# Kernel optimization log

Hardware: AMD Instinct MI355X
Metric: run time of the kernel (lower is better)

The kernel has to match this reference:

```python
import jax, jax.numpy as jnp
import numpy as np

B, IN_CH, OUT_CH, K, W_DIM, H = 16, 512, 512, 3, 512, 32


def setup_inputs() -> dict:
    key = jax.random.key(0)
    k1, k2, k3, k4 = jax.random.split(key, 4)
    return {
        "x": jax.random.normal(k1, (B, IN_CH, H, H), dtype=jnp.float32),
        "w": jax.random.normal(k2, (B, W_DIM), dtype=jnp.float32),
        "weight": jax.random.normal(k3, (1, OUT_CH, IN_CH, K, K), dtype=jnp.float32),
        "lin_w": jax.random.normal(k4, (IN_CH, W_DIM), dtype=jnp.float32),
        "lin_b": jnp.zeros((IN_CH,), dtype=jnp.float32),
    }


def reference(x, w, weight, lin_w, lin_b):
    k = weight.shape[-1]
    in_ch = weight.shape[2]
    fan_in = in_ch * k * k
    # equalized lr scaling of conv weight
    wt = weight * np.float32(np.sqrt(2.0 / fan_in))  # (1, out, in, k, k)
    # EqualizedLinear style: s = w @ (lin_w * sqrt(2/w_dim)).T + b
    s = w @ (lin_w * np.float32(np.sqrt(2.0 / lin_w.shape[1]))).T + lin_b  # (B, in)
    # modulate
    wm = s[:, None, :, None, None] * wt  # (B, out, in, k, k)
    # demodulate
    denom = jnp.sqrt(jnp.sum(wm * wm, axis=(2, 3, 4), keepdims=True) + 1e-8)
    wm = wm / denom
    # torch conv_transpose2d(stride=2, padding=0) == conv with lhs_dilation=2,
    # padding k-1 each side, spatially flipped kernel in OIHW layout.
    wflip = jnp.flip(wm, axis=(-2, -1))  # (B, out, in, k, k)

    def conv1(xi, wi):
        # xi: (in, h, w), wi: (out, in, k, k)
        return jax.lax.conv_general_dilated(
            xi[None], wi, window_strides=(1, 1),
            padding=[(k - 1, k - 1), (k - 1, k - 1)],
            lhs_dilation=(2, 2),
            dimension_numbers=("NCHW", "OIHW", "NCHW"))[0]

    out = jax.vmap(conv1)(x, wflip)  # (B, out, 2h+1, 2w+1)
    return out
```

## Files before the change

kernel.cpp:

```cpp
#include <hip/hip_runtime.h>
#include <hip/hip_bf16.h>


typedef __attribute__((ext_vector_type(8))) short short8;
typedef __attribute__((ext_vector_type(4))) float floatx4;

#define CIN   512
#define COUT  512
#define OW    65
#define NSITE 1089
#define XSLOT 1312

__device__ __forceinline__ void gload16(const void* g, void* l) {
    __builtin_amdgcn_global_load_lds(
        (const __attribute__((address_space(1))) void*)g,
        (__attribute__((address_space(3))) void*)l, 16, 0, 0);
}

template <int N>
__device__ __forceinline__ void vmwait() {
    asm volatile("s_waitcnt vmcnt(%0)" :: "n"(N) : "memory");
}


__global__ void k_s(const float* __restrict__ w, const float* __restrict__ lin_w,
                    const float* __restrict__ lin_b, float* __restrict__ s)
{
    int li = threadIdx.x >> 3, sl = threadIdx.x & 7;
    int i  = blockIdx.x * 32 + li;
    int b  = blockIdx.y;
    const float* wr = w + b * 512 + sl * 64;
    const float* lr = lin_w + (size_t)i * 512 + sl * 64;
    float acc = 0.f;
#pragma unroll
    for (int d = 0; d < 64; d += 4) {
        float4 a = *(const float4*)(wr + d);
        float4 c = *(const float4*)(lr + d);
        acc += a.x*c.x + a.y*c.y + a.z*c.z + a.w*c.w;
    }
    acc += __shfl_down(acc, 4, 8);
    acc += __shfl_down(acc, 2, 8);
    acc += __shfl_down(acc, 1, 8);
    if (sl == 0) s[b * 512 + i] = acc * 0.0625f + lin_b[i];
}

__global__ void k_wq(const float* __restrict__ weight,
                     __hip_bfloat16* __restrict__ wTf, float* __restrict__ q)
{
    int idx = blockIdx.x * 256 + threadIdx.x;
    int o = idx >> 9, i = idx & 511;
    const float* p = weight + (size_t)idx * 9;
    float v[9], acc = 0.f;
#pragma unroll
    for (int j = 0; j < 9; ++j) { v[j] = p[j]; acc += v[j] * v[j]; }
    q[idx] = acc;
    const int o32 = o >> 5, a = (o >> 4) & 1;
    const int kc = i >> 5, quad = (i >> 3) & 3;
    const size_t lanepos = ((size_t)(quad * 16 + (o & 15))) * 8 + (i & 7);
#pragma unroll
    for (int t = 0; t < 9; ++t)
        wTf[(((size_t)(t * 16 + o32) * 16 + kc) * 2 + a) * 512 + lanepos] =
            __float2bfloat16(v[t] * (1.0f / 48.0f));
}

__global__ void k_inv(const float* __restrict__ s, const float* __restrict__ q,
                      float* __restrict__ inv)
{
    int lo = threadIdx.x >> 3, sl = threadIdx.x & 7;
    int o  = blockIdx.x * 32 + lo;
    int b  = blockIdx.y;
    const float* sp = s + b * 512 + sl * 64;
    const float* qp = q + (size_t)o * 512 + sl * 64;
    float acc = 0.f;
#pragma unroll
    for (int i = 0; i < 64; i += 4) {
        float4 sv = *(const float4*)(sp + i);
        float4 qv = *(const float4*)(qp + i);
        acc += sv.x*sv.x*qv.x + sv.y*sv.y*qv.y + sv.z*sv.z*qv.z + sv.w*sv.w*qv.w;
    }
    acc += __shfl_down(acc, 4, 8);
    acc += __shfl_down(acc, 2, 8);
    acc += __shfl_down(acc, 1, 8);
    if (sl == 0)
        inv[b * 512 + o] = 1.0f / sqrtf(acc * (1.0f / 2304.0f) + 1e-8f);
}

__global__ void k_zero(__hip_bfloat16* __restrict__ xmp2)
{
    int idx = blockIdx.x * 256 + threadIdx.x;
    int q4 = idx & 3;
    int t  = idx >> 2;
    int si = t % 288;
    int bk = t / 288;
    int slot;
    if      (si < 34)  slot = si;
    else if (si < 68)  slot = 33 * 34 + (si - 34);
    else if (si < 100) slot = (si - 68 + 1) * 34;
    else if (si < 132) slot = (si - 100 + 1) * 34 + 33;
    else               slot = 1156 + (si - 132);
    uint4 z = {0u, 0u, 0u, 0u};
    *(uint4*)(xmp2 + ((size_t)bk * XSLOT + slot) * 32 + q4 * 8) = z;
}

__global__ void k_xprep(const float* __restrict__ x, const float* __restrict__ s,
                        __hip_bfloat16* __restrict__ xmp2)
{
    __shared__ float tile[32][33];
    int kc = blockIdx.x;
    int h  = blockIdx.y;
    int b  = blockIdx.z;
    int tw = threadIdx.x & 31;
    int ti = threadIdx.x >> 5;
#pragma unroll
    for (int r = 0; r < 4; ++r) {
        int il = ti + r * 8;
        int i  = kc * 32 + il;
        tile[il][tw] = x[(((size_t)b * 512 + i) * 32 + h) * 32 + tw] * s[b * 512 + i];
    }
    __syncthreads();
#pragma unroll
    for (int r = 0; r < 4; ++r) {
        int wc   = ti + r * 8;
        int slot = (h + 1) * 34 + (wc + 1);
        int pos  = (((tw >> 3) ^ ((slot >> 1) & 3)) << 3) | (tw & 7);
        xmp2[((size_t)(b * 16 + kc) * XSLOT + slot) * 32 + pos] =
            __float2bfloat16(tile[tw][wc]);
    }
}


template <int PY> struct PT;
template <> struct PT<0> {
    static constexpr int NT = 6, NG = 4;
    static constexpr int TAPL[6] = {0, 1, 2, 6, 7, 8};
    static constexpr int GTS[4]  = {35, 34, 1, 0};
    static constexpr int GSZ[4]  = {2, 1, 2, 1};
    static constexpr int GST[4]  = {0, 2, 3, 5};
    static constexpr int GPX[6]  = {0, 1, 0, 0, 1, 0};
    static constexpr int VM(int kc) {
        return kc == 0 ? 32 : kc <= 13 ? 44 : kc == 14 ? 40 : 24;
    }
};
template <> struct PT<1> {
    static constexpr int NT = 3, NG = 2;
    static constexpr int TAPL[3] = {3, 4, 5};
    static constexpr int GTS[2]  = {35, 34};
    static constexpr int GSZ[2]  = {2, 1};
    static constexpr int GST[2]  = {0, 2};
    static constexpr int GPX[3]  = {0, 1, 0};
    static constexpr int VM(int kc) {
        return kc == 0 ? 20 : kc <= 13 ? 26 : kc == 14 ? 22 : 12;
    }
};

#define STAGE_X(NB, KCI)                                                   \
    { _Pragma("unroll")                                                    \
      for (int it = 0; it < 4; ++it)                                       \
          gload16(xg[it] + (size_t)(KCI) * (XSLOT * 32),                   \
                  &Xl[(NB) + it * 2048 + wub]); }

#define PREFETCH_A(DST, KCI)                                               \
    { _Pragma("unroll")                                                    \
      for (int t = 0; t < NT; ++t) {                                       \
          Ar[DST][t][0] = *(const short8*)(wtapP[t] + (KCI) * 1024);       \
          Ar[DST][t][1] = *(const short8*)(wtapP[t] + (KCI) * 1024 + 512); \
      } }

#define COMPUTE_GROUPS(CB, CUR)                                            \
    { _Pragma("unroll")                                                    \
      for (int g = 0; g < NG; ++g) {                                       \
          short8 B0 = *(const short8*)(&Xl[(CB) + boff[g][0]]);            \
          short8 B1 = *(const short8*)(&Xl[(CB) + boff[g][1]]);            \
          short8 B2 = *(const short8*)(&Xl[(CB) + boff[g][2]]);            \
          short8 B3 = *(const short8*)(&Xl[(CB) + boff[g][3]]);            \
          _Pragma("unroll")                                                \
          for (int j = 0; j < T::GSZ[g]; ++j) {                            \
              const int ti = T::GST[g] + j;                                \
              const int px = T::GPX[ti];                                   \
              acc[px][0][0] = __builtin_amdgcn_mfma_f32_16x16x32_bf16(Ar[CUR][ti][0], B0, acc[px][0][0], 0, 0, 0); \
              acc[px][1][0] = __builtin_amdgcn_mfma_f32_16x16x32_bf16(Ar[CUR][ti][1], B0, acc[px][1][0], 0, 0, 0); \
              acc[px][0][1] = __builtin_amdgcn_mfma_f32_16x16x32_bf16(Ar[CUR][ti][0], B1, acc[px][0][1], 0, 0, 0); \
              acc[px][1][1] = __builtin_amdgcn_mfma_f32_16x16x32_bf16(Ar[CUR][ti][1], B1, acc[px][1][1], 0, 0, 0); \
              acc[px][0][2] = __builtin_amdgcn_mfma_f32_16x16x32_bf16(Ar[CUR][ti][0], B2, acc[px][0][2], 0, 0, 0); \
              acc[px][1][2] = __builtin_amdgcn_mfma_f32_16x16x32_bf16(Ar[CUR][ti][1], B2, acc[px][1][2], 0, 0, 0); \
              acc[px][0][3] = __builtin_amdgcn_mfma_f32_16x16x32_bf16(Ar[CUR][ti][0], B3, acc[px][0][3], 0, 0, 0); \
              acc[px][1][3] = __builtin_amdgcn_mfma_f32_16x16x32_bf16(Ar[CUR][ti][1], B3, acc[px][1][3], 0, 0, 0); \
          }                                                                \
      } }

#define CHUNK(KC, DO_STAGE, DO_A)                                          \
    { asm volatile("s_waitcnt lgkmcnt(0)" ::: "memory");                   \
      __builtin_amdgcn_s_barrier();                                        \
      if (DO_STAGE) STAGE_X((((KC) + 2) % 3) * 8192, (KC) + 2)             \
      if (DO_A)     PREFETCH_A(((KC) + 1) & 1, (KC) + 1)                   \
      vmwait<T::VM(KC)>();                                                 \
      __builtin_amdgcn_s_barrier();                                        \
      __builtin_amdgcn_s_setprio(1);                                       \
      COMPUTE_GROUPS(((KC) % 3) * 8192, (KC) & 1)                          \
      __builtin_amdgcn_s_setprio(0); }

template <int PY>
__device__ __forceinline__ void conv_body(
    const __hip_bfloat16* __restrict__ wTf,
    const __hip_bfloat16* __restrict__ xmp2,
    const float* __restrict__ inv,
    float* __restrict__ out,
    short* Xl, const int site_tile, const int o_tile, const int b)
{
    using T = PT<PY>;
    constexpr int NT = T::NT, NG = T::NG;

    const int tid  = threadIdx.x;
    const int lane = tid & 63;
    const int wv   = tid >> 6;
    const int wm   = wv & 1;
    const int wn   = wv >> 1;
    const int quad = lane >> 4;
    const int c16  = lane & 15;

    const int s0     = site_tile * 128;
    const int u_base = s0 / 33;
    const int o_base = o_tile * 64;
    const int o32    = o_tile * 2 + wm;

    const __hip_bfloat16* wtapP[NT];
#pragma unroll
    for (int t = 0; t < NT; ++t)
        wtapP[t] = wTf + (size_t)(T::TAPL[t] * 16 + o32) * 16384 + lane * 8;

    int boff[NG][4];
#pragma unroll
    for (int f = 0; f < 4; ++f) {
        int site = s0 + wn * 64 + f * 16 + c16;
        int u = site / 33;
        int v = site - u * 33;
        int sb = (u - u_base) * 34 + v;
#pragma unroll
        for (int g = 0; g < NG; ++g) {
            int sl = sb + T::GTS[g];
            int sg = sl + u_base * 34;
            boff[g][f] = sl * 32 + ((quad ^ ((sg >> 1) & 3)) << 3);
        }
    }
    const __hip_bfloat16* xb =
        xmp2 + ((size_t)b * 16 * XSLOT + (size_t)u_base * 34) * 32;
    const __hip_bfloat16* xg[4];
#pragma unroll
    for (int it = 0; it < 4; ++it)
        xg[it] = xb + (size_t)(it * 256 + tid) * 8;
    const int wub = (tid & 192) * 8;

    floatx4 acc[2][2][4];
#pragma unroll
    for (int p = 0; p < 2; ++p)
#pragma unroll
        for (int a = 0; a < 2; ++a)
#pragma unroll
            for (int f = 0; f < 4; ++f)
                acc[p][a][f] = (floatx4){0.f, 0.f, 0.f, 0.f};

    short8 Ar[2][NT][2];

    STAGE_X(0, 0)
    STAGE_X(8192, 1)
    PREFETCH_A(0, 0)

    CHUNK( 0, 1, 1)  CHUNK( 1, 1, 1)  CHUNK( 2, 1, 1)  CHUNK( 3, 1, 1)
    CHUNK( 4, 1, 1)  CHUNK( 5, 1, 1)  CHUNK( 6, 1, 1)  CHUNK( 7, 1, 1)
    CHUNK( 8, 1, 1)  CHUNK( 9, 1, 1)  CHUNK(10, 1, 1)  CHUNK(11, 1, 1)
    CHUNK(12, 1, 1)  CHUNK(13, 1, 1)  CHUNK(14, 0, 1)  CHUNK(15, 0, 0)

#pragma unroll
    for (int a = 0; a < 2; ++a) {
        const int ob = o_base + wm * 32 + a * 16 + quad * 4;
        float iv[4];
#pragma unroll
        for (int r = 0; r < 4; ++r) iv[r] = inv[b * COUT + ob + r];
#pragma unroll
        for (int f = 0; f < 4; ++f) {
            int site = s0 + wn * 64 + f * 16 + c16;
            if (site < NSITE) {
                int u = site / 33;
                int v = site - u * 33;
                int y = 2 * u + PY;
                if (y < OW) {
                    int x0 = 2 * v;
#pragma unroll
                    for (int r = 0; r < 4; ++r) {
                        size_t oi = ((size_t)(b * COUT + ob + r) * OW + y) * OW + x0;
                        out[oi] = acc[0][a][f][r] * iv[r];
                        if (v < 32)
                            out[oi + 1] = acc[1][a][f][r] * iv[r];
                    }
                }
            }
        }
    }
}

__global__ __launch_bounds__(256, 2)
void conv_main(const __hip_bfloat16* __restrict__ wTf,
               const __hip_bfloat16* __restrict__ xmp2,
               const float* __restrict__ inv,
               float* __restrict__ out)
{
    __shared__ short Xl[24576];

    const int n  = blockIdx.x + 9 * blockIdx.y + 144 * blockIdx.z;
    const int lg = (n & 7) * 288 + (n >> 3);
    const int b  = lg / 144;
    int rem = lg - b * 144;
    const int o_tile = rem / 18;
    rem -= o_tile * 18;
    const int py   = rem / 9;
    const int site = rem - py * 9;

    if (py == 0) conv_body<0>(wTf, xmp2, inv, out, Xl, site, o_tile, b);
    else         conv_body<1>(wTf, xmp2, inv, out, Xl, site, o_tile, b);
}

extern "C" void kernel_launch(void* const* d_in, const int* in_sizes, int n_in,
                              void* d_out, int out_size, void* d_ws, size_t ws_size,
                              hipStream_t stream)
{
    const float* x      = (const float*)d_in[0];
    const float* w      = (const float*)d_in[1];
    const float* weight = (const float*)d_in[2];
    const float* lin_w  = (const float*)d_in[3];
    const float* lin_b  = (const float*)d_in[4];
    float* out = (float*)d_out;

    char* ws = (char*)d_ws;
    float* s_buf   = (float*)(ws);
    float* inv_buf = (float*)(ws + 32768);
    float* q_buf   = (float*)(ws + 65536);
    __hip_bfloat16* wTf  = (__hip_bfloat16*)(ws + 1114112);
    __hip_bfloat16* xmp2 = (__hip_bfloat16*)(ws + 5832704);

    k_s    <<<dim3(16, 16),     256, 0, stream>>>(w, lin_w, lin_b, s_buf);
    k_wq   <<<1024,             256, 0, stream>>>(weight, wTf, q_buf);
    k_zero <<<1152,             256, 0, stream>>>(xmp2);
    k_inv  <<<dim3(16, 16),     256, 0, stream>>>(s_buf, q_buf, inv_buf);
    k_xprep<<<dim3(16, 32, 16), 256, 0, stream>>>(x, s_buf, xmp2);
    conv_main<<<dim3(9, 16, 16), 256, 0, stream>>>(wTf, xmp2, inv_buf, out);
}
```

Measured before the change: 287.8 us.

## Merge prep kernels, single-buffer A fragments with split prefetch, raise occupancy

Five small prep kernels are merged into two launches, with blocks dispatched by index range, to cut launch overhead. In the conv kernel the double-buffered A register fragments become a single buffer. The next chunk's A loads are split into two halves, each issued after the compute group that last uses those taps. Launch bounds rise from 2 to 3 blocks per SIMD to improve latency hiding, with vmcnt waits retuned to match. The risks are register spills under the tighter bound and exposed A-load latency, since loads now arrive later relative to their use.

```diff
diff --git a/kernel.cpp b/kernel.cpp
--- a/kernel.cpp
+++ b/kernel.cpp
@@ -23,12 +23,13 @@
 }
 
 
-__global__ void k_s(const float* __restrict__ w, const float* __restrict__ lin_w,
-                    const float* __restrict__ lin_b, float* __restrict__ s)
-{
-    int li = threadIdx.x >> 3, sl = threadIdx.x & 7;
-    int i  = blockIdx.x * 32 + li;
-    int b  = blockIdx.y;
+__device__ __forceinline__ void d_s(int blk, int tid,
+    const float* __restrict__ w, const float* __restrict__ lin_w,
+    const float* __restrict__ lin_b, float* __restrict__ s)
+{
+    int li = tid >> 3, sl = tid & 7;
+    int i  = (blk & 15) * 32 + li;
+    int b  = blk >> 4;
     const float* wr = w + b * 512 + sl * 64;
     const float* lr = lin_w + (size_t)i * 512 + sl * 64;
     float acc = 0.f;
@@ -44,10 +45,11 @@
     if (sl == 0) s[b * 512 + i] = acc * 0.0625f + lin_b[i];
 }
 
-__global__ void k_wq(const float* __restrict__ weight,
-                     __hip_bfloat16* __restrict__ wTf, float* __restrict__ q)
-{
-    int idx = blockIdx.x * 256 + threadIdx.x;
+__device__ __forceinline__ void d_wq(int blk, int tid,
+    const float* __restrict__ weight, __hip_bfloat16* __restrict__ wTf,
+    float* __restrict__ q)
+{
+    int idx = blk * 256 + tid;
     int o = idx >> 9, i = idx & 511;
     const float* p = weight + (size_t)idx * 9;
     float v[9], acc = 0.f;
@@ -63,31 +65,10 @@
             __float2bfloat16(v[t] * (1.0f / 48.0f));
 }
 
-__global__ void k_inv(const float* __restrict__ s, const float* __restrict__ q,
-                      float* __restrict__ inv)
-{
-    int lo = threadIdx.x >> 3, sl = threadIdx.x & 7;
-    int o  = blockIdx.x * 32 + lo;
-    int b  = blockIdx.y;
-    const float* sp = s + b * 512 + sl * 64;
-    const float* qp = q + (size_t)o * 512 + sl * 64;
-    float acc = 0.f;
-#pragma unroll
-    for (int i = 0; i < 64; i += 4) {
-        float4 sv = *(const float4*)(sp + i);
-        float4 qv = *(const float4*)(qp + i);
-        acc += sv.x*sv.x*qv.x + sv.y*sv.y*qv.y + sv.z*sv.z*qv.z + sv.w*sv.w*qv.w;
-    }
-    acc += __shfl_down(acc, 4, 8);
-    acc += __shfl_down(acc, 2, 8);
-    acc += __shfl_down(acc, 1, 8);
-    if (sl == 0)
-        inv[b * 512 + o] = 1.0f / sqrtf(acc * (1.0f / 2304.0f) + 1e-8f);
-}
-
-__global__ void k_zero(__hip_bfloat16* __restrict__ xmp2)
-{
-    int idx = blockIdx.x * 256 + threadIdx.x;
+__device__ __forceinline__ void d_zero(int blk, int tid,
+    __hip_bfloat16* __restrict__ xmp2)
+{
+    int idx = blk * 256 + tid;
     int q4 = idx & 3;
     int t  = idx >> 2;
     int si = t % 288;
@@ -102,15 +83,54 @@
     *(uint4*)(xmp2 + ((size_t)bk * XSLOT + slot) * 32 + q4 * 8) = z;
 }
 
-__global__ void k_xprep(const float* __restrict__ x, const float* __restrict__ s,
-                        __hip_bfloat16* __restrict__ xmp2)
+__device__ __forceinline__ void d_inv(int blk, int tid,
+    const float* __restrict__ s, const float* __restrict__ q,
+    float* __restrict__ inv)
+{
+    int lo = tid >> 3, sl = tid & 7;
+    int o  = (blk & 15) * 32 + lo;
+    int b  = blk >> 4;
+    const float* sp = s + b * 512 + sl * 64;
+    const float* qp = q + (size_t)o * 512 + sl * 64;
+    float acc = 0.f;
+#pragma unroll
+    for (int i = 0; i < 64; i += 4) {
+        float4 sv = *(const float4*)(sp + i);
+        float4 qv = *(const float4*)(qp + i);
+        acc += sv.x*sv.x*qv.x + sv.y*sv.y*qv.y + sv.z*sv.z*qv.z + sv.w*sv.w*qv.w;
+    }
+    acc += __shfl_down(acc, 4, 8);
+    acc += __shfl_down(acc, 2, 8);
+    acc += __shfl_down(acc, 1, 8);
+    if (sl == 0)
+        inv[b * 512 + o] = 1.0f / sqrtf(acc * (1.0f / 2304.0f) + 1e-8f);
+}
+
+
+__global__ void prep_a(const float* __restrict__ w, const float* __restrict__ lin_w,
+                       const float* __restrict__ lin_b, const float* __restrict__ weight,
+                       float* __restrict__ s, __hip_bfloat16* __restrict__ wTf,
+                       float* __restrict__ q, __hip_bfloat16* __restrict__ xmp2)
+{
+    int blk = blockIdx.x, tid = threadIdx.x;
+    if      (blk < 256)  d_s   (blk,        tid, w, lin_w, lin_b, s);
+    else if (blk < 1280) d_wq  (blk - 256,  tid, weight, wTf, q);
+    else                 d_zero(blk - 1280, tid, xmp2);
+}
+
+__global__ void prep_b(const float* __restrict__ x, const float* __restrict__ s,
+                       const float* __restrict__ q, float* __restrict__ inv,
+                       __hip_bfloat16* __restrict__ xmp2)
 {
     __shared__ float tile[32][33];
-    int kc = blockIdx.x;
-    int h  = blockIdx.y;
-    int b  = blockIdx.z;
-    int tw = threadIdx.x & 31;
-    int ti = threadIdx.x >> 5;
+    int blk = blockIdx.x, tid = threadIdx.x;
+    if (blk < 256) { d_inv(blk, tid, s, q, inv); return; }
+    int id = blk - 256;
+    int kc = id & 15;
+    int h  = (id >> 4) & 31;
+    int b  = id >> 9;
+    int tw = tid & 31;
+    int ti = tid >> 5;
 #pragma unroll
     for (int r = 0; r < 4; ++r) {
         int il = ti + r * 8;
@@ -131,25 +151,25 @@
 
 template <int PY> struct PT;
 template <> struct PT<0> {
-    static constexpr int NT = 6, NG = 4;
+    static constexpr int NT = 6, NG = 4, NGH = 2, TH = 3;
     static constexpr int TAPL[6] = {0, 1, 2, 6, 7, 8};
     static constexpr int GTS[4]  = {35, 34, 1, 0};
     static constexpr int GSZ[4]  = {2, 1, 2, 1};
     static constexpr int GST[4]  = {0, 2, 3, 5};
     static constexpr int GPX[6]  = {0, 1, 0, 0, 1, 0};
     static constexpr int VM(int kc) {
-        return kc == 0 ? 32 : kc <= 13 ? 44 : kc == 14 ? 40 : 24;
+        return kc == 0 ? 20 : kc <= 13 ? 32 : kc == 14 ? 28 : 24;
     }
 };
 template <> struct PT<1> {
-    static constexpr int NT = 3, NG = 2;
+    static constexpr int NT = 3, NG = 2, NGH = 1, TH = 2;
     static constexpr int TAPL[3] = {3, 4, 5};
     static constexpr int GTS[2]  = {35, 34};
     static constexpr int GSZ[2]  = {2, 1};
     static constexpr int GST[2]  = {0, 2};
     static constexpr int GPX[3]  = {0, 1, 0};
     static constexpr int VM(int kc) {
-        return kc == 0 ? 20 : kc <= 13 ? 26 : kc == 14 ? 22 : 12;
+        return kc == 0 ? 14 : kc <= 13 ? 20 : kc == 14 ? 16 : 12;
     }
 };
 
@@ -159,16 +179,16 @@
           gload16(xg[it] + (size_t)(KCI) * (XSLOT * 32),                   \
                   &Xl[(NB) + it * 2048 + wub]); }
 
-#define PREFETCH_A(DST, KCI)                                               \
+#define PREFETCH_A(TLO, THI, KCI)                                          \
     { _Pragma("unroll")                                                    \
-      for (int t = 0; t < NT; ++t) {                                       \
-          Ar[DST][t][0] = *(const short8*)(wtapP[t] + (KCI) * 1024);       \
-          Ar[DST][t][1] = *(const short8*)(wtapP[t] + (KCI) * 1024 + 512); \
+      for (int t = (TLO); t < (THI); ++t) {                                \
+          Ar[t][0] = *(const short8*)(wtapP[t] + (KCI) * 1024);            \
+          Ar[t][1] = *(const short8*)(wtapP[t] + (KCI) * 1024 + 512);      \
       } }
 
-#define COMPUTE_GROUPS(CB, CUR)                                            \
+#define COMPUTE_RANGE(CB, GLO, GHI)                                        \
     { _Pragma("unroll")                                                    \
-      for (int g = 0; g < NG; ++g) {                                       \
+      for (int g = (GLO); g < (GHI); ++g) {                                \
           short8 B0 = *(const short8*)(&Xl[(CB) + boff[g][0]]);            \
           short8 B1 = *(const short8*)(&Xl[(CB) + boff[g][1]]);            \
           short8 B2 = *(const short8*)(&Xl[(CB) + boff[g][2]]);            \
@@ -177,14 +197,14 @@
           for (int j = 0; j < T::GSZ[g]; ++j) {                            \
               const int ti = T::GST[g] + j;                                \
               const int px = T::GPX[ti];                                   \
-              acc[px][0][0] = __builtin_amdgcn_mfma_f32_16x16x32_bf16(Ar[CUR][ti][0], B0, acc[px][0][0], 0, 0, 0); \
-              acc[px][1][0] = __builtin_amdgcn_mfma_f32_16x16x32_bf16(Ar[CUR][ti][1], B0, acc[px][1][0], 0, 0, 0); \
-              acc[px][0][1] = __builtin_amdgcn_mfma_f32_16x16x32_bf16(Ar[CUR][ti][0], B1, acc[px][0][1], 0, 0, 0); \
-              acc[px][1][1] = __builtin_amdgcn_mfma_f32_16x16x32_bf16(Ar[CUR][ti][1], B1, acc[px][1][1], 0, 0, 0); \
-              acc[px][0][2] = __builtin_amdgcn_mfma_f32_16x16x32_bf16(Ar[CUR][ti][0], B2, acc[px][0][2], 0, 0, 0); \
-              acc[px][1][2] = __builtin_amdgcn_mfma_f32_16x16x32_bf16(Ar[CUR][ti][1], B2, acc[px][1][2], 0, 0, 0); \
-              acc[px][0][3] = __builtin_amdgcn_mfma_f32_16x16x32_bf16(Ar[CUR][ti][0], B3, acc[px][0][3], 0, 0, 0); \
-              acc[px][1][3] = __builtin_amdgcn_mfma_f32_16x16x32_bf16(Ar[CUR][ti][1], B3, acc[px][1][3], 0, 0, 0); \
+              acc[px][0][0] = __builtin_amdgcn_mfma_f32_16x16x32_bf16(Ar[ti][0], B0, acc[px][0][0], 0, 0, 0); \
+              acc[px][1][0] = __builtin_amdgcn_mfma_f32_16x16x32_bf16(Ar[ti][1], B0, acc[px][1][0], 0, 0, 0); \
+              acc[px][0][1] = __builtin_amdgcn_mfma_f32_16x16x32_bf16(Ar[ti][0], B1, acc[px][0][1], 0, 0, 0); \
+              acc[px][1][1] = __builtin_amdgcn_mfma_f32_16x16x32_bf16(Ar[ti][1], B1, acc[px][1][1], 0, 0, 0); \
+              acc[px][0][2] = __builtin_amdgcn_mfma_f32_16x16x32_bf16(Ar[ti][0], B2, acc[px][0][2], 0, 0, 0); \
+              acc[px][1][2] = __builtin_amdgcn_mfma_f32_16x16x32_bf16(Ar[ti][1], B2, acc[px][1][2], 0, 0, 0); \
+              acc[px][0][3] = __builtin_amdgcn_mfma_f32_16x16x32_bf16(Ar[ti][0], B3, acc[px][0][3], 0, 0, 0); \
+              acc[px][1][3] = __builtin_amdgcn_mfma_f32_16x16x32_bf16(Ar[ti][1], B3, acc[px][1][3], 0, 0, 0); \
           }                                                                \
       } }
 
@@ -192,12 +212,16 @@
     { asm volatile("s_waitcnt lgkmcnt(0)" ::: "memory");                   \
       __builtin_amdgcn_s_barrier();                                        \
       if (DO_STAGE) STAGE_X((((KC) + 2) % 3) * 8192, (KC) + 2)             \
-      if (DO_A)     PREFETCH_A(((KC) + 1) & 1, (KC) + 1)                   \
       vmwait<T::VM(KC)>();                                                 \
       __builtin_amdgcn_s_barrier();                                        \
       __builtin_amdgcn_s_setprio(1);                                       \
-      COMPUTE_GROUPS(((KC) % 3) * 8192, (KC) & 1)                          \
-      __builtin_amdgcn_s_setprio(0); }
+      COMPUTE_RANGE(((KC) % 3) * 8192, 0, T::NGH)                          \
+      __builtin_amdgcn_s_setprio(0);                                       \
+      if (DO_A) PREFETCH_A(0, T::TH, (KC) + 1)                             \
+      __builtin_amdgcn_s_setprio(1);                                       \
+      COMPUTE_RANGE(((KC) % 3) * 8192, T::NGH, NG)                         \
+      __builtin_amdgcn_s_setprio(0);                                       \
+      if (DO_A) PREFETCH_A(T::TH, NT, (KC) + 1) }
 
 template <int PY>
 __device__ __forceinline__ void conv_body(
@@ -259,11 +283,11 @@
             for (int f = 0; f < 4; ++f)
                 acc[p][a][f] = (floatx4){0.f, 0.f, 0.f, 0.f};
 
-    short8 Ar[2][NT][2];
+    short8 Ar[NT][2];
 
     STAGE_X(0, 0)
     STAGE_X(8192, 1)
-    PREFETCH_A(0, 0)
+    PREFETCH_A(0, NT, 0)
 
     CHUNK( 0, 1, 1)  CHUNK( 1, 1, 1)  CHUNK( 2, 1, 1)  CHUNK( 3, 1, 1)
     CHUNK( 4, 1, 1)  CHUNK( 5, 1, 1)  CHUNK( 6, 1, 1)  CHUNK( 7, 1, 1)
@@ -298,7 +322,7 @@
     }
 }
 
-__global__ __launch_bounds__(256, 2)
+__global__ __launch_bounds__(256, 3)
 void conv_main(const __hip_bfloat16* __restrict__ wTf,
                const __hip_bfloat16* __restrict__ xmp2,
                const float* __restrict__ inv,
@@ -337,10 +361,7 @@
     __hip_bfloat16* wTf  = (__hip_bfloat16*)(ws + 1114112);
     __hip_bfloat16* xmp2 = (__hip_bfloat16*)(ws + 5832704);
 
-    k_s    <<<dim3(16, 16),     256, 0, stream>>>(w, lin_w, lin_b, s_buf);
-    k_wq   <<<1024,             256, 0, stream>>>(weight, wTf, q_buf);
-    k_zero <<<1152,             256, 0, stream>>>(xmp2);
-    k_inv  <<<dim3(16, 16),     256, 0, stream>>>(s_buf, q_buf, inv_buf);
-    k_xprep<<<dim3(16, 32, 16), 256, 0, stream>>>(x, s_buf, xmp2);
+    prep_a<<<2432, 256, 0, stream>>>(w, lin_w, lin_b, weight, s_buf, wTf, q_buf, xmp2);
+    prep_b<<<8448, 256, 0, stream>>>(x, s_buf, q_buf, inv_buf, xmp2);
     conv_main<<<dim3(9, 16, 16), 256, 0, stream>>>(wTf, xmp2, inv_buf, out);
 }
```

Result: slower. 321.9 us (+11.8%).
